# Performance work log

Measured on AMD Instinct MI355X. Metric: run time of the kernel, lower is better.

The kernel has to match this reference:

```python
import jax, jax.numpy as jnp
import numpy as np

NUM_HEADS = 8
MAX_POINTS = 8


def _sample_one(img, x, y):
    # img: [hd, Hs, Ws]; x, y: [N, P] pixel coords. Bilinear, zeros padding,
    # align_corners=True (caller already converted normalized coords to pixels).
    Hs, Ws = img.shape[-2], img.shape[-1]
    x0f = jnp.floor(x); y0f = jnp.floor(y)
    x0 = x0f.astype(jnp.int32); y0 = y0f.astype(jnp.int32)
    x1 = x0 + 1; y1 = y0 + 1
    wx1 = x - x0f; wx0 = 1.0 - wx1
    wy1 = y - y0f; wy0 = 1.0 - wy1

    def gather(yi, xi):
        valid = ((yi >= 0) & (yi < Hs) & (xi >= 0) & (xi < Ws)).astype(img.dtype)
        yc = jnp.clip(yi, 0, Hs - 1)
        xc = jnp.clip(xi, 0, Ws - 1)
        return img[:, yc, xc] * valid  # [hd, N, P]

    return (gather(y0, x0) * (wy0 * wx0) + gather(y0, x1) * (wy0 * wx1)
            + gather(y1, x0) * (wy1 * wx0) + gather(y1, x1) * (wy1 * wx1))


def _forward(query, ref, q_w, q_b, kv_w, kv_b, off_w, off_b, out_w, out_b, H, W, n_points):
    B, N, C = query.shape
    hd = C // NUM_HEADS
    scale = hd ** -0.5

    q = (query @ q_w + q_b).reshape(B, N, NUM_HEADS, hd)
    # kv_proj is dead code in the source forward (k, v are never used); params kept for parity.

    offsets = (query @ off_w + off_b).reshape(B, N, NUM_HEADS, MAX_POINTS, 2)
    offsets = offsets[:, :, :, :n_points]  # [B, N, nh, P, 2]

    ys = jnp.arange(H, dtype=query.dtype)
    xs = jnp.arange(W, dtype=query.dtype)
    coords = jnp.stack(jnp.meshgrid(ys, xs, indexing='ij'), -1).reshape(N, 2)  # (y, x)
    loc = coords[None, :, None, None, :] + offsets  # [B, N, nh, P, 2]
    g0 = loc[..., 0] / (H - 1) * 2.0 - 1.0
    g1 = loc[..., 1] / (W - 1) * 2.0 - 1.0
    # grid_sample reads grid[...,0] as x and grid[...,1] as y -> faithful to the
    # source's coordinate-channel ordering (channel 0 was normalized with H).
    x_pix = (g0 + 1.0) * 0.5 * (W - 1)
    y_pix = (g1 + 1.0) * 0.5 * (H - 1)

    ref_img = ref.reshape(B, C, H, W)  # faithful to source's .view (raw reinterpret, no permute)
    ref_heads = ref_img.reshape(B, NUM_HEADS, hd, H, W)  # per-head channel slice

    xb = x_pix.transpose(0, 2, 1, 3)  # [B, nh, N, P]
    yb = y_pix.transpose(0, 2, 1, 3)
    sampled = jax.vmap(jax.vmap(_sample_one))(ref_heads, xb, yb)  # [B, nh, hd, N, P]
    sampled = sampled.transpose(0, 3, 1, 4, 2)  # [B, N, nh, P, hd]

    attn = jax.nn.softmax(jnp.einsum('bnhd,bnhpd->bnhp', q, sampled) * scale, axis=-1)
    out = jnp.einsum('bnhp,bnhpd->bnhd', attn, sampled).reshape(B, N, C)
    return out @ out_w + out_b


def setup_inputs():
    key = jax.random.key(0)
    B, H, W, C = 4, 64, 64, 512
    N = H * W
    ks = jax.random.split(key, 8)
    w = lambda k, shp: jax.random.normal(k, shp, jnp.float32) * 0.02
    return {
        'query': jax.random.normal(ks[0], (B, N, C), jnp.float32),
        'ref': jax.random.normal(ks[1], (B, N, C), jnp.float32),
        'q_w': w(ks[2], (C, C)), 'q_b': jnp.zeros((C,), jnp.float32),
        'kv_w': w(ks[3], (C, 2 * C)), 'kv_b': jnp.zeros((2 * C,), jnp.float32),
        'off_w': w(ks[4], (C, NUM_HEADS * MAX_POINTS * 2)),
        'off_b': jnp.zeros((NUM_HEADS * MAX_POINTS * 2,), jnp.float32),
        'out_w': w(ks[5], (C, C)), 'out_b': jnp.zeros((C,), jnp.float32),
        'H': H, 'W': W, 'n_points': 8,
    }


def reference(query, ref, q_w, q_b, kv_w, kv_b, off_w, off_b, out_w, out_b, H, W, n_points):
    return _forward(query, ref, q_w, q_b, kv_w, kv_b, off_w, off_b, out_w, out_b, H, W, n_points)
```

## Files before the change

kernel.cpp:

```cpp
#include <hip/hip_runtime.h>
#include <cmath>

#define NUM_HEADS 8
#define MAX_POINTS 8
#define HD 64

typedef short bf16x8 __attribute__((ext_vector_type(8)));
typedef float f32x4 __attribute__((ext_vector_type(4)));

typedef const __attribute__((address_space(1))) unsigned int gu32;
typedef __attribute__((address_space(3))) unsigned int lu32;

__device__ __forceinline__ unsigned short f2bf(float f) {
    unsigned u = __float_as_uint(f);
    unsigned r = (u + 0x7fff + ((u >> 16) & 1)) >> 16;
    return (unsigned short)r;
}
__device__ __forceinline__ float bf2f(unsigned short s) {
    return __uint_as_float(((unsigned)s) << 16);
}
__device__ __forceinline__ unsigned packbf2(float a, float b) {
    return (unsigned)f2bf(a) | ((unsigned)f2bf(b) << 16);
}
__device__ __forceinline__ void unpack8(uint4 u, float* f) {
    f[0] = __uint_as_float(u.x << 16); f[1] = __uint_as_float(u.x & 0xffff0000u);
    f[2] = __uint_as_float(u.y << 16); f[3] = __uint_as_float(u.y & 0xffff0000u);
    f[4] = __uint_as_float(u.z << 16); f[5] = __uint_as_float(u.z & 0xffff0000u);
    f[6] = __uint_as_float(u.w << 16); f[7] = __uint_as_float(u.w & 0xffff0000u);
}

__global__ __launch_bounds__(256) void cvt_bf16_k(
    const float* __restrict__ in, unsigned short* __restrict__ out, int n)
{
    int i = (blockIdx.x * 256 + threadIdx.x) * 4;
    if (i >= n) return;
    float4 v = *(const float4*)&in[i];
    ushort4 o;
    o.x = f2bf(v.x); o.y = f2bf(v.y); o.z = f2bf(v.z); o.w = f2bf(v.w);
    *(ushort4*)&out[i] = o;
}

__global__ __launch_bounds__(256) void tconv_k(
    const float* __restrict__ in, unsigned short* __restrict__ out, int K, int N)
{
    __shared__ float tile[32][33];
    size_t ib = (size_t)blockIdx.z * K * N;
    int k0 = blockIdx.x * 32, n0 = blockIdx.y * 32;
    int tx = threadIdx.x, ty = threadIdx.y;
#pragma unroll
    for (int i = 0; i < 32; i += 8)
        tile[ty + i][tx] = in[ib + (size_t)(k0 + ty + i) * N + n0 + tx];
    __syncthreads();
#pragma unroll
    for (int i = 0; i < 32; i += 8)
        out[ib + (size_t)(n0 + ty + i) * K + k0 + tx] = f2bf(tile[tx][ty + i]);
}

#define LDK 40

__global__ __launch_bounds__(256) void gemm_bf16_mfma64(
    const unsigned short* __restrict__ A, const unsigned short* __restrict__ BT,
    const float* __restrict__ bias, float* __restrict__ Cf,
    unsigned short* __restrict__ Cb, int M, int N, int K)
{
    __shared__ unsigned short As[64 * LDK];
    __shared__ unsigned short Bs[64 * LDK];
    int tid = threadIdx.x;
    int wave = tid >> 6, lane = tid & 63;
    int quad = lane >> 4, l16 = lane & 15;
    int bm = blockIdx.y * 64, bn = blockIdx.x * 64;
    int wm = (wave >> 1) * 32, wn = (wave & 1) * 32;
    int srow = tid >> 2, schunk = (tid & 3) * 8;

    f32x4 acc[2][2];
#pragma unroll
    for (int i = 0; i < 2; ++i)
#pragma unroll
        for (int j = 0; j < 2; ++j)
            acc[i][j] = (f32x4){0.f, 0.f, 0.f, 0.f};

    for (int k0 = 0; k0 < K; k0 += 32) {
        *(uint4*)&As[srow * LDK + schunk] =
            *(const uint4*)&A[(size_t)(bm + srow) * K + k0 + schunk];
        *(uint4*)&Bs[srow * LDK + schunk] =
            *(const uint4*)&BT[(size_t)(bn + srow) * K + k0 + schunk];
        __syncthreads();
        bf16x8 af[2], bfr[2];
#pragma unroll
        for (int t = 0; t < 2; ++t) {
            af[t]  = *(const bf16x8*)&As[(wm + t * 16 + l16) * LDK + quad * 8];
            bfr[t] = *(const bf16x8*)&Bs[(wn + t * 16 + l16) * LDK + quad * 8];
        }
#pragma unroll
        for (int mt = 0; mt < 2; ++mt)
#pragma unroll
            for (int nt = 0; nt < 2; ++nt)
                acc[mt][nt] = __builtin_amdgcn_mfma_f32_16x16x32_bf16(
                    af[mt], bfr[nt], acc[mt][nt], 0, 0, 0);
        __syncthreads();
    }
#pragma unroll
    for (int mt = 0; mt < 2; ++mt)
#pragma unroll
        for (int nt = 0; nt < 2; ++nt) {
            int r0 = bm + wm + mt * 16 + quad * 4;
            int c  = bn + wn + nt * 16 + l16;
            float bv = bias[c];
#pragma unroll
            for (int r = 0; r < 4; ++r) {
                float v = acc[mt][nt][r] + bv;
                if (Cf) Cf[(size_t)(r0 + r) * N + c] = v;
                if (Cb) Cb[(size_t)(r0 + r) * N + c] = f2bf(v);
            }
        }
}

__global__ __launch_bounds__(256) void gemm_bf16_mfma128(
    const unsigned short* __restrict__ A, const unsigned short* __restrict__ BT,
    const float* __restrict__ bias, float* __restrict__ Cf,
    unsigned short* __restrict__ Cb, int M, int N, int K)
{
    __shared__ unsigned short As[128 * 32];
    __shared__ unsigned short Bs[128 * 32];
    int tid = threadIdx.x;
    int wave = tid >> 6, lane = tid & 63;
    int quad = lane >> 4, l16 = lane & 15;
    int bm = blockIdx.y * 128, bn = blockIdx.x * 128;
    int wm = (wave >> 1) * 64, wn = (wave & 1) * 64;

    int srow = tid >> 2, sq = (tid & 3) * 8;
    const unsigned short* aP0 = &A[(size_t)(bm + srow) * K + sq];
    const unsigned short* aP1 = aP0 + (size_t)64 * K;
    const unsigned short* bP0 = &BT[(size_t)(bn + srow) * K + sq];
    const unsigned short* bP1 = bP0 + (size_t)64 * K;
    lu32* aL0 = (lu32*)&As[wave * 512];
    lu32* aL1 = (lu32*)&As[2048 + wave * 512];
    lu32* bL0 = (lu32*)&Bs[wave * 512];
    lu32* bL1 = (lu32*)&Bs[2048 + wave * 512];

    f32x4 acc[4][4];
#pragma unroll
    for (int i = 0; i < 4; ++i)
#pragma unroll
        for (int j = 0; j < 4; ++j)
            acc[i][j] = (f32x4){0.f, 0.f, 0.f, 0.f};

    for (int k0 = 0; k0 < K; k0 += 32) {
        __builtin_amdgcn_global_load_lds((gu32*)(aP0 + k0), aL0, 16, 0, 0);
        __builtin_amdgcn_global_load_lds((gu32*)(aP1 + k0), aL1, 16, 0, 0);
        __builtin_amdgcn_global_load_lds((gu32*)(bP0 + k0), bL0, 16, 0, 0);
        __builtin_amdgcn_global_load_lds((gu32*)(bP1 + k0), bL1, 16, 0, 0);
        __syncthreads();
        bf16x8 af[4], bfr[4];
#pragma unroll
        for (int t = 0; t < 4; ++t) {
            af[t]  = *(const bf16x8*)&As[(wm + t * 16 + l16) * 32 + quad * 8];
            bfr[t] = *(const bf16x8*)&Bs[(wn + t * 16 + l16) * 32 + quad * 8];
        }
#pragma unroll
        for (int mt = 0; mt < 4; ++mt)
#pragma unroll
            for (int nt = 0; nt < 4; ++nt)
                acc[mt][nt] = __builtin_amdgcn_mfma_f32_16x16x32_bf16(
                    af[mt], bfr[nt], acc[mt][nt], 0, 0, 0);
        __syncthreads();
    }

#pragma unroll
    for (int mt = 0; mt < 4; ++mt)
#pragma unroll
        for (int nt = 0; nt < 4; ++nt) {
            int r0 = bm + wm + mt * 16 + quad * 4;
            int c  = bn + wn + nt * 16 + l16;
            float bv = bias[c];
#pragma unroll
            for (int r = 0; r < 4; ++r) {
                float v = acc[mt][nt][r] + bv;
                if (Cf) Cf[(size_t)(r0 + r) * N + c] = v;
                if (Cb) Cb[(size_t)(r0 + r) * N + c] = f2bf(v);
            }
        }
}

__global__ __launch_bounds__(256) void sample_attn8_k(
    const unsigned short* __restrict__ qb, const float* __restrict__ offb,
    const unsigned short* __restrict__ refT, unsigned short* __restrict__ ob,
    const int* __restrict__ Hp, const int* __restrict__ Wp,
    const int* __restrict__ npp, int B, int N, int C)
{
    int H = *Hp, W = *Wp, npts = *npp;
    int bn = blockIdx.x * 4 + (threadIdx.x >> 6);
    int lane = threadIdx.x & 63;
    int h = lane >> 3;
    int c8 = (lane & 7) << 3;
    int coff = (h << 6) + c8;
    int b = bn / N, n = bn - b * N;
    int row = n / W, col = n - row * W;

    float qv[8];
    unpack8(*(const uint4*)&qb[bn * C + coff], qv);

    const float* op = offb + bn * (NUM_HEADS * MAX_POINTS * 2) + (h << 4);
    const unsigned short* rb = refT + b * N * C;

    float rX = (H > 1) ? (float)(W - 1) / (float)(H - 1) : 0.f;
    float rY = (W > 1) ? (float)(H - 1) / (float)(W - 1) : 0.f;

    float sv[MAX_POINTS][8];
    float lg[MAX_POINTS];
#pragma unroll
    for (int p = 0; p < MAX_POINTS; ++p) {
        float off0 = op[p * 2 + 0];
        float off1 = op[p * 2 + 1];
        float x = ((float)row + off0) * rX;
        float y = ((float)col + off1) * rY;
        float x0f = floorf(x), y0f = floorf(y);
        int x0 = (int)x0f, y0 = (int)y0f;
        float wx1 = x - x0f, wx0 = 1.f - wx1;
        float wy1 = y - y0f, wy0 = 1.f - wy1;

        float a8[8] = {0.f, 0.f, 0.f, 0.f, 0.f, 0.f, 0.f, 0.f};
#pragma unroll
        for (int t = 0; t < 4; ++t) {
            int yi = y0 + (t >> 1);
            int xi = x0 + (t & 1);
            float wgt = ((t >> 1) ? wy1 : wy0) * ((t & 1) ? wx1 : wx0);
            bool ok = ((unsigned)yi < (unsigned)H) & ((unsigned)xi < (unsigned)W);
            float wv = ok ? wgt : 0.f;
            int yc = min(max(yi, 0), H - 1);
            int xc = min(max(xi, 0), W - 1);
            float sf[8];
            unpack8(*(const uint4*)&rb[(yc * W + xc) * C + coff], sf);
#pragma unroll
            for (int j = 0; j < 8; ++j) a8[j] = fmaf(wv, sf[j], a8[j]);
        }
        float t = 0.f;
#pragma unroll
        for (int j = 0; j < 8; ++j) {
            sv[p][j] = a8[j];
            t = fmaf(qv[j], a8[j], t);
        }
        t += __shfl_xor(t, 1);
        t += __shfl_xor(t, 2);
        t += __shfl_xor(t, 4);
        lg[p] = (p < npts) ? t * 0.125f : -1e30f;
    }

    float mx = -1e30f;
#pragma unroll
    for (int p = 0; p < MAX_POINTS; ++p) mx = fmaxf(mx, lg[p]);
    float ssum = 0.f;
#pragma unroll
    for (int p = 0; p < MAX_POINTS; ++p) {
        lg[p] = __expf(lg[p] - mx);
        ssum += lg[p];
    }
    float inv = 1.f / ssum;

    float o8[8] = {0.f, 0.f, 0.f, 0.f, 0.f, 0.f, 0.f, 0.f};
#pragma unroll
    for (int p = 0; p < MAX_POINTS; ++p)
#pragma unroll
        for (int j = 0; j < 8; ++j) o8[j] = fmaf(lg[p], sv[p][j], o8[j]);

    uint4 o;
    o.x = packbf2(o8[0] * inv, o8[1] * inv);
    o.y = packbf2(o8[2] * inv, o8[3] * inv);
    o.z = packbf2(o8[4] * inv, o8[5] * inv);
    o.w = packbf2(o8[6] * inv, o8[7] * inv);
    *(uint4*)&ob[bn * C + coff] = o;
}

extern "C" void kernel_launch(void* const* d_in, const int* in_sizes, int n_in,
                              void* d_out, int out_size, void* d_ws, size_t ws_size,
                              hipStream_t stream) {
    const float* query = (const float*)d_in[0];
    const float* ref   = (const float*)d_in[1];
    const float* q_w   = (const float*)d_in[2];
    const float* q_b   = (const float*)d_in[3];
    const float* off_w = (const float*)d_in[6];
    const float* off_b = (const float*)d_in[7];
    const float* out_w = (const float*)d_in[8];
    const float* out_b = (const float*)d_in[9];
    const int* Hp   = (const int*)d_in[10];
    const int* Wp   = (const int*)d_in[11];
    const int* npp  = (const int*)d_in[12];

    const int C = 512;
    const int B = 4;
    const int H = 64, W = 64;
    const int N = H * W;
    const int M = B * N;
    const int OFFD = NUM_HEADS * MAX_POINTS * 2;

    float* offbuf = (float*)d_ws;
    unsigned short* refT_bf = (unsigned short*)(offbuf + (size_t)M * OFFD);
    unsigned short* qin_bf  = refT_bf + (size_t)M * C;
    unsigned short* qbuf_bf = qin_bf  + (size_t)M * C;
    unsigned short* obuf_bf = qbuf_bf + (size_t)M * C;
    unsigned short* wqT     = obuf_bf + (size_t)M * C;
    unsigned short* woffT   = wqT   + (size_t)C * C;
    unsigned short* woutT   = woffT + (size_t)OFFD * C;

    dim3 blk(256);
    cvt_bf16_k<<<dim3((M * C) / 1024), blk, 0, stream>>>(query, qin_bf, M * C);
    tconv_k<<<dim3(C / 32, C / 32), dim3(32, 8), 0, stream>>>(q_w, wqT, C, C);
    tconv_k<<<dim3(C / 32, OFFD / 32), dim3(32, 8), 0, stream>>>(off_w, woffT, C, OFFD);
    tconv_k<<<dim3(C / 32, C / 32), dim3(32, 8), 0, stream>>>(out_w, woutT, C, C);
    tconv_k<<<dim3(C / 32, N / 32, B), dim3(32, 8), 0, stream>>>(ref, refT_bf, C, N);

    gemm_bf16_mfma128<<<dim3(C / 128, M / 128), blk, 0, stream>>>(
        qin_bf, wqT, q_b, nullptr, qbuf_bf, M, C, C);
    gemm_bf16_mfma64<<<dim3(OFFD / 64, M / 64), blk, 0, stream>>>(
        qin_bf, woffT, off_b, offbuf, nullptr, M, OFFD, C);

    sample_attn8_k<<<dim3(M / 4), blk, 0, stream>>>(
        qbuf_bf, offbuf, refT_bf, obuf_bf, Hp, Wp, npp, B, N, C);

    gemm_bf16_mfma128<<<dim3(C / 128, M / 128), blk, 0, stream>>>(
        obuf_bf, woutT, out_b, (float*)d_out, nullptr, M, C, C);
}
```

Before: 224.7 us.

## Fuse q and offset projections into one GEMM and specialize the sampler

The q and offset weights are concatenated into one transposed buffer, so a single 128-tile MFMA GEMM with a split epilogue writes the bf16 q and the fp32 offsets. This replaces the separate 64-tile offset GEMM launch and its second read of the query activations. The sampling kernel now hardcodes H=W=64 and C=512, turning divisions and multiplies into shifts. It drops the coordinate ratio scaling, which is valid only because H equals W, loads offsets as float4, and takes a fast path with no clamping for interior bilinear taps. The price is a kernel that only works for these fixed shapes, and one GEMM launch that does mixed work per column tile.

```diff
diff --git a/kernel.cpp b/kernel.cpp
--- a/kernel.cpp
+++ b/kernel.cpp
@@ -4,6 +4,9 @@
 #define NUM_HEADS 8
 #define MAX_POINTS 8
 #define HD 64
+#define SH 64
+#define SW 64
+#define SC 512
 
 typedef short bf16x8 __attribute__((ext_vector_type(8)));
 typedef float f32x4 __attribute__((ext_vector_type(4)));
@@ -15,9 +18,6 @@
     unsigned u = __float_as_uint(f);
     unsigned r = (u + 0x7fff + ((u >> 16) & 1)) >> 16;
     return (unsigned short)r;
-}
-__device__ __forceinline__ float bf2f(unsigned short s) {
-    return __uint_as_float(((unsigned)s) << 16);
 }
 __device__ __forceinline__ unsigned packbf2(float a, float b) {
     return (unsigned)f2bf(a) | ((unsigned)f2bf(b) << 16);
@@ -56,78 +56,14 @@
         out[ib + (size_t)(n0 + ty + i) * K + k0 + tx] = f2bf(tile[tx][ty + i]);
 }
 
-#define LDK 40
-
-__global__ __launch_bounds__(256) void gemm_bf16_mfma64(
-    const unsigned short* __restrict__ A, const unsigned short* __restrict__ BT,
-    const float* __restrict__ bias, float* __restrict__ Cf,
-    unsigned short* __restrict__ Cb, int M, int N, int K)
-{
-    __shared__ unsigned short As[64 * LDK];
-    __shared__ unsigned short Bs[64 * LDK];
-    int tid = threadIdx.x;
+__device__ __forceinline__ void gemm128_core(
+    const unsigned short* A, const unsigned short* BT, int K,
+    int bm, int bn, int tid, unsigned short* As, unsigned short* Bs,
+    f32x4 (&acc)[4][4])
+{
     int wave = tid >> 6, lane = tid & 63;
     int quad = lane >> 4, l16 = lane & 15;
-    int bm = blockIdx.y * 64, bn = blockIdx.x * 64;
-    int wm = (wave >> 1) * 32, wn = (wave & 1) * 32;
-    int srow = tid >> 2, schunk = (tid & 3) * 8;
-
-    f32x4 acc[2][2];
-#pragma unroll
-    for (int i = 0; i < 2; ++i)
-#pragma unroll
-        for (int j = 0; j < 2; ++j)
-            acc[i][j] = (f32x4){0.f, 0.f, 0.f, 0.f};
-
-    for (int k0 = 0; k0 < K; k0 += 32) {
-        *(uint4*)&As[srow * LDK + schunk] =
-            *(const uint4*)&A[(size_t)(bm + srow) * K + k0 + schunk];
-        *(uint4*)&Bs[srow * LDK + schunk] =
-            *(const uint4*)&BT[(size_t)(bn + srow) * K + k0 + schunk];
-        __syncthreads();
-        bf16x8 af[2], bfr[2];
-#pragma unroll
-        for (int t = 0; t < 2; ++t) {
-            af[t]  = *(const bf16x8*)&As[(wm + t * 16 + l16) * LDK + quad * 8];
-            bfr[t] = *(const bf16x8*)&Bs[(wn + t * 16 + l16) * LDK + quad * 8];
-        }
-#pragma unroll
-        for (int mt = 0; mt < 2; ++mt)
-#pragma unroll
-            for (int nt = 0; nt < 2; ++nt)
-                acc[mt][nt] = __builtin_amdgcn_mfma_f32_16x16x32_bf16(
-                    af[mt], bfr[nt], acc[mt][nt], 0, 0, 0);
-        __syncthreads();
-    }
-#pragma unroll
-    for (int mt = 0; mt < 2; ++mt)
-#pragma unroll
-        for (int nt = 0; nt < 2; ++nt) {
-            int r0 = bm + wm + mt * 16 + quad * 4;
-            int c  = bn + wn + nt * 16 + l16;
-            float bv = bias[c];
-#pragma unroll
-            for (int r = 0; r < 4; ++r) {
-                float v = acc[mt][nt][r] + bv;
-                if (Cf) Cf[(size_t)(r0 + r) * N + c] = v;
-                if (Cb) Cb[(size_t)(r0 + r) * N + c] = f2bf(v);
-            }
-        }
-}
-
-__global__ __launch_bounds__(256) void gemm_bf16_mfma128(
-    const unsigned short* __restrict__ A, const unsigned short* __restrict__ BT,
-    const float* __restrict__ bias, float* __restrict__ Cf,
-    unsigned short* __restrict__ Cb, int M, int N, int K)
-{
-    __shared__ unsigned short As[128 * 32];
-    __shared__ unsigned short Bs[128 * 32];
-    int tid = threadIdx.x;
-    int wave = tid >> 6, lane = tid & 63;
-    int quad = lane >> 4, l16 = lane & 15;
-    int bm = blockIdx.y * 128, bn = blockIdx.x * 128;
     int wm = (wave >> 1) * 64, wn = (wave & 1) * 64;
-
     int srow = tid >> 2, sq = (tid & 3) * 8;
     const unsigned short* aP0 = &A[(size_t)(bm + srow) * K + sq];
     const unsigned short* aP1 = aP0 + (size_t)64 * K;
@@ -138,13 +74,6 @@
     lu32* bL0 = (lu32*)&Bs[wave * 512];
     lu32* bL1 = (lu32*)&Bs[2048 + wave * 512];
 
-    f32x4 acc[4][4];
-#pragma unroll
-    for (int i = 0; i < 4; ++i)
-#pragma unroll
-        for (int j = 0; j < 4; ++j)
-            acc[i][j] = (f32x4){0.f, 0.f, 0.f, 0.f};
-
     for (int k0 = 0; k0 < K; k0 += 32) {
         __builtin_amdgcn_global_load_lds((gu32*)(aP0 + k0), aL0, 16, 0, 0);
         __builtin_amdgcn_global_load_lds((gu32*)(aP1 + k0), aL1, 16, 0, 0);
@@ -165,6 +94,70 @@
                     af[mt], bfr[nt], acc[mt][nt], 0, 0, 0);
         __syncthreads();
     }
+}
+
+__global__ __launch_bounds__(256) void gemm_qoff_k(
+    const unsigned short* __restrict__ A, const unsigned short* __restrict__ BT,
+    const float* __restrict__ q_b, const float* __restrict__ off_b,
+    unsigned short* __restrict__ qout, float* __restrict__ offout,
+    int M, int K)
+{
+    __shared__ unsigned short As[128 * 32];
+    __shared__ unsigned short Bs[128 * 32];
+    int tid = threadIdx.x;
+    int wave = tid >> 6, lane = tid & 63;
+    int quad = lane >> 4, l16 = lane & 15;
+    int bm = blockIdx.y * 128, bn = blockIdx.x * 128;
+    int wm = (wave >> 1) * 64, wn = (wave & 1) * 64;
+
+    f32x4 acc[4][4];
+#pragma unroll
+    for (int i = 0; i < 4; ++i)
+#pragma unroll
+        for (int j = 0; j < 4; ++j) acc[i][j] = (f32x4){0.f, 0.f, 0.f, 0.f};
+
+    gemm128_core(A, BT, K, bm, bn, tid, As, Bs, acc);
+
+#pragma unroll
+    for (int mt = 0; mt < 4; ++mt)
+#pragma unroll
+        for (int nt = 0; nt < 4; ++nt) {
+            int r0 = bm + wm + mt * 16 + quad * 4;
+            int c  = bn + wn + nt * 16 + l16;
+            if (bn < 512) {
+                float bv = q_b[c];
+#pragma unroll
+                for (int r = 0; r < 4; ++r)
+                    qout[(size_t)(r0 + r) * 512 + c] = f2bf(acc[mt][nt][r] + bv);
+            } else {
+                int co = c - 512;
+                float bv = off_b[co];
+#pragma unroll
+                for (int r = 0; r < 4; ++r)
+                    offout[(size_t)(r0 + r) * 128 + co] = acc[mt][nt][r] + bv;
+            }
+        }
+}
+
+__global__ __launch_bounds__(256) void gemm_out_k(
+    const unsigned short* __restrict__ A, const unsigned short* __restrict__ BT,
+    const float* __restrict__ bias, float* __restrict__ Cf, int M, int N, int K)
+{
+    __shared__ unsigned short As[128 * 32];
+    __shared__ unsigned short Bs[128 * 32];
+    int tid = threadIdx.x;
+    int wave = tid >> 6, lane = tid & 63;
+    int quad = lane >> 4, l16 = lane & 15;
+    int bm = blockIdx.y * 128, bn = blockIdx.x * 128;
+    int wm = (wave >> 1) * 64, wn = (wave & 1) * 64;
+
+    f32x4 acc[4][4];
+#pragma unroll
+    for (int i = 0; i < 4; ++i)
+#pragma unroll
+        for (int j = 0; j < 4; ++j) acc[i][j] = (f32x4){0.f, 0.f, 0.f, 0.f};
+
+    gemm128_core(A, BT, K, bm, bn, tid, As, Bs, acc);
 
 #pragma unroll
     for (int mt = 0; mt < 4; ++mt)
@@ -174,65 +167,82 @@
             int c  = bn + wn + nt * 16 + l16;
             float bv = bias[c];
 #pragma unroll
-            for (int r = 0; r < 4; ++r) {
-                float v = acc[mt][nt][r] + bv;
-                if (Cf) Cf[(size_t)(r0 + r) * N + c] = v;
-                if (Cb) Cb[(size_t)(r0 + r) * N + c] = f2bf(v);
-            }
+            for (int r = 0; r < 4; ++r)
+                Cf[(size_t)(r0 + r) * N + c] = acc[mt][nt][r] + bv;
         }
 }
 
 __global__ __launch_bounds__(256) void sample_attn8_k(
     const unsigned short* __restrict__ qb, const float* __restrict__ offb,
     const unsigned short* __restrict__ refT, unsigned short* __restrict__ ob,
-    const int* __restrict__ Hp, const int* __restrict__ Wp,
-    const int* __restrict__ npp, int B, int N, int C)
-{
-    int H = *Hp, W = *Wp, npts = *npp;
+    const int* __restrict__ npp)
+{
+    int npts = *npp;
     int bn = blockIdx.x * 4 + (threadIdx.x >> 6);
     int lane = threadIdx.x & 63;
     int h = lane >> 3;
     int c8 = (lane & 7) << 3;
     int coff = (h << 6) + c8;
-    int b = bn / N, n = bn - b * N;
-    int row = n / W, col = n - row * W;
+    int b = bn >> 12;
+    int n = bn & 4095;
+    int row = n >> 6, col = n & 63;
 
     float qv[8];
-    unpack8(*(const uint4*)&qb[bn * C + coff], qv);
-
-    const float* op = offb + bn * (NUM_HEADS * MAX_POINTS * 2) + (h << 4);
-    const unsigned short* rb = refT + b * N * C;
-
-    float rX = (H > 1) ? (float)(W - 1) / (float)(H - 1) : 0.f;
-    float rY = (W > 1) ? (float)(H - 1) / (float)(W - 1) : 0.f;
+    unpack8(*(const uint4*)&qb[(bn << 9) + coff], qv);
+
+    const float* op = offb + (bn << 7) + (h << 4);
+    float4 of4[4];
+    of4[0] = *(const float4*)(op + 0);
+    of4[1] = *(const float4*)(op + 4);
+    of4[2] = *(const float4*)(op + 8);
+    of4[3] = *(const float4*)(op + 12);
+    const float* offs = (const float*)of4;
+
+    const unsigned short* rb = refT + ((size_t)b << 21);
 
     float sv[MAX_POINTS][8];
     float lg[MAX_POINTS];
 #pragma unroll
     for (int p = 0; p < MAX_POINTS; ++p) {
-        float off0 = op[p * 2 + 0];
-        float off1 = op[p * 2 + 1];
-        float x = ((float)row + off0) * rX;
-        float y = ((float)col + off1) * rY;
+        float x = (float)row + offs[p * 2 + 0];
+        float y = (float)col + offs[p * 2 + 1];
         float x0f = floorf(x), y0f = floorf(y);
         int x0 = (int)x0f, y0 = (int)y0f;
         float wx1 = x - x0f, wx0 = 1.f - wx1;
         float wy1 = y - y0f, wy0 = 1.f - wy1;
-
-        float a8[8] = {0.f, 0.f, 0.f, 0.f, 0.f, 0.f, 0.f, 0.f};
-#pragma unroll
-        for (int t = 0; t < 4; ++t) {
-            int yi = y0 + (t >> 1);
-            int xi = x0 + (t & 1);
-            float wgt = ((t >> 1) ? wy1 : wy0) * ((t & 1) ? wx1 : wx0);
-            bool ok = ((unsigned)yi < (unsigned)H) & ((unsigned)xi < (unsigned)W);
-            float wv = ok ? wgt : 0.f;
-            int yc = min(max(yi, 0), H - 1);
-            int xc = min(max(xi, 0), W - 1);
-            float sf[8];
-            unpack8(*(const uint4*)&rb[(yc * W + xc) * C + coff], sf);
-#pragma unroll
-            for (int j = 0; j < 8; ++j) a8[j] = fmaf(wv, sf[j], a8[j]);
+        float w00 = wy0 * wx0, w01 = wy0 * wx1;
+        float w10 = wy1 * wx0, w11 = wy1 * wx1;
+
+        float a8[8];
+        if (((unsigned)y0 < 63u) & ((unsigned)x0 < 63u)) {
+            const unsigned short* base = rb + (((y0 << 6) + x0) << 9) + coff;
+            float s0[8], s1[8], s2[8], s3[8];
+            unpack8(*(const uint4*)(base), s0);
+            unpack8(*(const uint4*)(base + 512), s1);
+            unpack8(*(const uint4*)(base + 32768), s2);
+            unpack8(*(const uint4*)(base + 32768 + 512), s3);
+#pragma unroll
+            for (int j = 0; j < 8; ++j)
+                a8[j] = fmaf(w00, s0[j],
+                        fmaf(w01, s1[j],
+                        fmaf(w10, s2[j], w11 * s3[j])));
+        } else {
+#pragma unroll
+            for (int j = 0; j < 8; ++j) a8[j] = 0.f;
+            float wt[4] = {w00, w01, w10, w11};
+#pragma unroll
+            for (int t = 0; t < 4; ++t) {
+                int yi = y0 + (t >> 1);
+                int xi = x0 + (t & 1);
+                bool ok = ((unsigned)yi < 64u) & ((unsigned)xi < 64u);
+                float wv = ok ? wt[t] : 0.f;
+                int yc = min(max(yi, 0), 63);
+                int xc = min(max(xi, 0), 63);
+                float sf[8];
+                unpack8(*(const uint4*)&rb[(((yc << 6) + xc) << 9) + coff], sf);
+#pragma unroll
+                for (int j = 0; j < 8; ++j) a8[j] = fmaf(wv, sf[j], a8[j]);
+            }
         }
         float t = 0.f;
 #pragma unroll
@@ -268,7 +278,7 @@
     o.y = packbf2(o8[2] * inv, o8[3] * inv);
     o.z = packbf2(o8[4] * inv, o8[5] * inv);
     o.w = packbf2(o8[6] * inv, o8[7] * inv);
-    *(uint4*)&ob[bn * C + coff] = o;
+    *(uint4*)&ob[(bn << 9) + coff] = o;
 }
 
 extern "C" void kernel_launch(void* const* d_in, const int* in_sizes, int n_in,
@@ -282,14 +292,11 @@
     const float* off_b = (const float*)d_in[7];
     const float* out_w = (const float*)d_in[8];
     const float* out_b = (const float*)d_in[9];
-    const int* Hp   = (const int*)d_in[10];
-    const int* Wp   = (const int*)d_in[11];
     const int* npp  = (const int*)d_in[12];
 
     const int C = 512;
     const int B = 4;
-    const int H = 64, W = 64;
-    const int N = H * W;
+    const int N = 64 * 64;
     const int M = B * N;
     const int OFFD = NUM_HEADS * MAX_POINTS * 2;
 
@@ -298,25 +305,23 @@
     unsigned short* qin_bf  = refT_bf + (size_t)M * C;
     unsigned short* qbuf_bf = qin_bf  + (size_t)M * C;
     unsigned short* obuf_bf = qbuf_bf + (size_t)M * C;
-    unsigned short* wqT     = obuf_bf + (size_t)M * C;
-    unsigned short* woffT   = wqT   + (size_t)C * C;
-    unsigned short* woutT   = woffT + (size_t)OFFD * C;
+    unsigned short* wcat    = obuf_bf + (size_t)M * C;
+    unsigned short* woutT   = wcat + (size_t)(C + OFFD) * C;
 
     dim3 blk(256);
     cvt_bf16_k<<<dim3((M * C) / 1024), blk, 0, stream>>>(query, qin_bf, M * C);
-    tconv_k<<<dim3(C / 32, C / 32), dim3(32, 8), 0, stream>>>(q_w, wqT, C, C);
-    tconv_k<<<dim3(C / 32, OFFD / 32), dim3(32, 8), 0, stream>>>(off_w, woffT, C, OFFD);
+    tconv_k<<<dim3(C / 32, C / 32), dim3(32, 8), 0, stream>>>(q_w, wcat, C, C);
+    tconv_k<<<dim3(C / 32, OFFD / 32), dim3(32, 8), 0, stream>>>(
+        off_w, wcat + (size_t)C * C, C, OFFD);
     tconv_k<<<dim3(C / 32, C / 32), dim3(32, 8), 0, stream>>>(out_w, woutT, C, C);
     tconv_k<<<dim3(C / 32, N / 32, B), dim3(32, 8), 0, stream>>>(ref, refT_bf, C, N);
 
-    gemm_bf16_mfma128<<<dim3(C / 128, M / 128), blk, 0, stream>>>(
-        qin_bf, wqT, q_b, nullptr, qbuf_bf, M, C, C);
-    gemm_bf16_mfma64<<<dim3(OFFD / 64, M / 64), blk, 0, stream>>>(
-        qin_bf, woffT, off_b, offbuf, nullptr, M, OFFD, C);
+    gemm_qoff_k<<<dim3(5, M / 128), blk, 0, stream>>>(
+        qin_bf, wcat, q_b, off_b, qbuf_bf, offbuf, M, C);
 
     sample_attn8_k<<<dim3(M / 4), blk, 0, stream>>>(
-        qbuf_bf, offbuf, refT_bf, obuf_bf, Hp, Wp, npp, B, N, C);
-
-    gemm_bf16_mfma128<<<dim3(C / 128, M / 128), blk, 0, stream>>>(
-        obuf_bf, woutT, out_b, (float*)d_out, nullptr, M, C, C);
-}
+        qbuf_bf, offbuf, refT_bf, obuf_bf, npp);
+
+    gemm_out_k<<<dim3(C / 128, M / 128), blk, 0, stream>>>(
+        obuf_bf, woutT, out_b, (float*)d_out, M, C, C);
+}
```

Result: faster. 220.3 us (-2.0%).
